# Kernel tuning notes

Hardware: AMD Instinct MI355X
Metric: run time of the kernel (lower is better)

## Reference

```python
import jax, jax.numpy as jnp
import numpy as np

B, T, NM = 128, 2048, 8  # batch, nSteps, nMaxwell


def setup_inputs() -> dict:
    key = jax.random.key(0)
    k1, k2, k3 = jax.random.split(key, 3)
    S_e = jax.random.normal(k1, (B, T, 3, 3), dtype=jnp.float32)
    # strictly increasing times per batch element
    dt = jax.random.uniform(k2, (B, T), minval=0.01, maxval=0.1, dtype=jnp.float32)
    t = jnp.cumsum(dt, axis=1)
    # [tau_1..tau_nM, g_infy, g_1..g_nM] -> last dim 2*NM + 1
    PronyParams = jax.random.uniform(k3, (B, T, 2 * NM + 1), minval=0.1, maxval=1.0, dtype=jnp.float32)
    return {"S_e": S_e, "t": t, "PronyParams": PronyParams}


def reference(S_e, t, PronyParams):
    """Viscoelastic 2nd Piola-Kirchhoff stress via recursive Prony update.

    S_e:         [B, T, 3, 3] instantaneous elastic stress
    t:           [B, T] time
    PronyParams: [B, T, 2*nM+1] (relaxation times tau then coefficients g)
    Returns (S, S_infy, Q_sum), each [B, T, 3, 3].
    """
    nM = PronyParams.shape[-1] // 2
    tau = PronyParams[..., :nM]                      # [B,T,nM]
    g = PronyParams[..., nM:]                        # [B,T,nM+1]
    g = g / jnp.sum(g, axis=-1, keepdims=True)
    g_infy = g[..., 0:1]                             # [B,T,1]
    g_i = g[..., 1:]                                 # [B,T,nM]

    Bsz = S_e.shape[0]
    # time-major scan inputs
    xs = (
        jnp.swapaxes(t, 0, 1),      # [T,B]
        jnp.swapaxes(S_e, 0, 1),    # [T,B,3,3]
        jnp.swapaxes(tau, 0, 1),    # [T,B,nM]
        jnp.swapaxes(g_i, 0, 1),    # [T,B,nM]
    )
    init = (
        jnp.zeros((Bsz, nM, 3, 3), S_e.dtype),  # Q_0
        -t[:, 1],                                # t_prev (as in original initializer)
        jnp.zeros((Bsz, 3, 3), S_e.dtype),       # S_prev
        tau[:, 0],
        g_i[:, 0],
    )

    def step(carry, x):
        Q_p, t_p, S_p, tau_p, g_p = carry
        t_c, S_c, tau_c, g_c = x
        g_bar = 0.5 * (g_c + g_p)                 # [B,nM]
        tau_bar = 0.5 * (tau_c + tau_p)           # [B,nM]
        dt = (t_c - t_p)[:, None]                 # [B,1]
        e = jnp.exp(-0.5 * dt / tau_bar)          # exp(-dt/(2 tau_bar))
        term1 = (e * e)[..., None, None]          # exp(-dt/tau_bar), [B,nM,1,1]
        term2 = (e * g_bar)[..., None, None]      # [B,nM,1,1]
        dS = (S_c - S_p)[:, None]                 # [B,1,3,3]
        Q = term1 * Q_p + term2 * dS              # [B,nM,3,3]
        return (Q, t_c, S_c, tau_c, g_c), Q

    _, Qs = jax.lax.scan(step, init, xs)          # [T,B,nM,3,3]
    Q_sum = jnp.swapaxes(jnp.sum(Qs, axis=2), 0, 1)  # [B,T,3,3]
    S_infy = g_infy[..., None] * S_e              # [B,T,1,1] * [B,T,3,3]
    S = S_infy + Q_sum
    return (S, S_infy, Q_sum)
```

## Files before the change

### kernel.cpp

```cpp
#include <hip/hip_runtime.h>

#define T_LEN 2048
#define NMODE 8
#define NPP   17

template <int L, int G>
__global__ __launch_bounds__(256, 8)
void aggK(const float* __restrict__ Se,
          const float* __restrict__ tt,
          const float* __restrict__ pp,
          float* __restrict__ agg,
          int B) {
    constexpr int NSTEP = G * L;
    constexpr int TILES = T_LEN / NSTEP;
    constexpr int RW    = NSTEP + 1;
    constexpr int NT    = 256;
    constexpr int AC_K  = L * 16 + 4;
    constexpr int OV_R  = 0;
    constexpr int OV_P  = G * 72;
    static_assert(OV_P + G * 8 <= G * AC_K, "overlay fits");
    constexpr int O_INV = G * AC_K;
    constexpr int TOTAL = O_INV + RW;

    __shared__ __align__(16) float sm[TOTAL];
    float* s_AC  = sm;
    float* s_R   = sm + OV_R;
    float* s_P   = sm + OV_P;
    float* s_inv = sm + O_INV;

    const int tid  = threadIdx.x;
    const int b    = blockIdx.x / (TILES - 1);
    const int tile = blockIdx.x % (TILES - 1);

    const int base = tile * NSTEP;
    const int off  = (base == 0) ? 0 : 1;
    const int r0   = (base == 0) ? 0 : base - 1;

    const float* ppb = pp + ((size_t)b * T_LEN + r0) * NPP;
    const float* ttb = tt + (size_t)b * T_LEN + r0;

    for (int i = tid; i < RW; i += NT) {
        const float* gp = ppb + i * NPP + 8;
        float gs = 0.f;
        #pragma unroll
        for (int k = 0; k < 9; ++k) gs += gp[k];
        s_inv[i] = __builtin_amdgcn_rcpf(gs);
    }
    __syncthreads();

    for (int i = tid; i < NSTEP * 8; i += NT) {
        int m  = i & 7;
        int ts = i >> 3;
        int rc = ts + off;
        bool first = (base == 0) && (ts == 0);
        int rp = first ? rc : rc - 1;
        float tau_c = ppb[rc * NPP + m];
        float tau_p = ppb[rp * NPP + m];
        float gqh_c = 0.5f * ppb[rc * NPP + 9 + m] * s_inv[rc];
        float gqh_p = 0.5f * ppb[rp * NPP + 9 + m] * s_inv[rp];
        float t_c = ttb[rc];
        float t_p = first ? -ttb[1] : ttb[rp];
        float ee  = __expf((t_p - t_c) * __builtin_amdgcn_rcpf(tau_c + tau_p));
        int kk = ts / L, sl = ts % L;
        s_AC[kk * AC_K + sl * 16 + m]     = ee * ee;
        s_AC[kk * AC_K + sl * 16 + 8 + m] = ee * (gqh_c + gqh_p);
    }
    __syncthreads();

    float Q[8] = {0,0,0,0,0,0,0,0};
    float cumA_c = 1.f;
    if (tid < 72) {
        const int k = tid / 9;
        const int e = tid - k * 9;
        const float* Sg = Se + (size_t)b * T_LEN * 9 + e;
        const int gbase = base + k * L;

        float dS[L];
        {
            float prev = (base == 0 && k == 0) ? 0.f
                                               : Sg[(size_t)(gbase - 1) * 9];
            #pragma unroll
            for (int s = 0; s < L; ++s) {
                float cur = Sg[(size_t)(gbase + s) * 9];
                dS[s] = cur - prev;
                prev = cur;
            }
        }

        const float4* acp = (const float4*)(s_AC + k * AC_K);
        #pragma unroll
        for (int s = 0; s < L; ++s) {
            float4 a0 = acp[4*s], a1 = acp[4*s+1];
            float4 c0v = acp[4*s+2], c1v = acp[4*s+3];
            float d = dS[s];
            Q[0] = a0.x*Q[0] + c0v.x*d;  Q[1] = a0.y*Q[1] + c0v.y*d;
            Q[2] = a0.z*Q[2] + c0v.z*d;  Q[3] = a0.w*Q[3] + c0v.w*d;
            Q[4] = a1.x*Q[4] + c1v.x*d;  Q[5] = a1.y*Q[5] + c1v.y*d;
            Q[6] = a1.z*Q[6] + c1v.z*d;  Q[7] = a1.w*Q[7] + c1v.w*d;
        }
    } else if (tid >= 192) {
        const int u = tid - 192;
        const int k = u >> 3;
        const int m = u & 7;
        #pragma unroll
        for (int s = 0; s < L; ++s)
            cumA_c *= s_AC[k * AC_K + s * 16 + m];
    }
    __syncthreads();

    if (tid < 72) {
        float4* r4 = (float4*)(s_R + 8 * tid);
        r4[0] = make_float4(Q[0], Q[1], Q[2], Q[3]);
        r4[1] = make_float4(Q[4], Q[5], Q[6], Q[7]);
    } else if (tid >= 192) {
        s_P[tid - 192] = cumA_c;
    }
    __syncthreads();

    if (tid < 72) {
        const int e = tid >> 3;
        const int m = tid & 7;
        float z = 0.f, pprod = 1.f;
        #pragma unroll
        for (int k = 0; k < G; ++k) {
            float Pk = s_P[k * 8 + m];
            z = Pk * z + s_R[k * 72 + tid];
            pprod *= Pk;
        }
        float* ap = agg + ((size_t)b * TILES + tile) * 80;
        ap[8 + tid] = z;
        if (e == 0) ap[m] = pprod;
    }
}

template <int L, int G>
__global__ __launch_bounds__(256, 8)
void finK(const float* __restrict__ Se,
          const float* __restrict__ tt,
          const float* __restrict__ pp,
          float* __restrict__ out,
          const float* __restrict__ agg,
          int B) {
    constexpr int NSTEP = G * L;
    constexpr int TILES = T_LEN / NSTEP;
    constexpr int RW    = NSTEP + 1;
    constexpr int NT    = 256;
    constexpr int SROW  = NSTEP + 4;
    constexpr int QT_SZ = 9 * SROW;
    constexpr int CA_K  = L * 8 + 4;
    constexpr int AC_K  = L * 16 + 4;
    constexpr int O_AC  = QT_SZ + G * CA_K;
    constexpr int OV_R  = 0;
    constexpr int OV_P  = G * 72;
    constexpr int OV_Z  = OV_P + G * 8;
    static_assert(OV_Z + G * 72 <= G * AC_K, "overlay fits");
    constexpr int O_INV = O_AC + G * AC_K;
    constexpr int O_GI  = O_INV + RW;
    constexpr int O_ZIN = O_GI + RW;
    constexpr int TOTAL = O_ZIN + 72;
    static_assert(TOTAL * 4 <= 20480, "LDS must allow 8 blocks/CU");
    static_assert(L == 16, "epilogue uses t>>4 / t&15");

    __shared__ __align__(16) float sm[TOTAL];
    float* s_qT  = sm;
    float* s_ca  = sm + QT_SZ;
    float* s_AC  = sm + O_AC;
    float* s_R   = sm + O_AC + OV_R;
    float* s_P   = sm + O_AC + OV_P;
    float* s_Z   = sm + O_AC + OV_Z;
    float* s_inv = sm + O_INV;
    float* s_gi  = sm + O_GI;
    float* s_Zin = sm + O_ZIN;

    const int tid  = threadIdx.x;
    const int b    = blockIdx.x / TILES;
    const int tile = blockIdx.x % TILES;

    const int base = tile * NSTEP;
    const int off  = (base == 0) ? 0 : 1;
    const int r0   = (base == 0) ? 0 : base - 1;

    const float* ppb = pp + ((size_t)b * T_LEN + r0) * NPP;
    const float* ttb = tt + (size_t)b * T_LEN + r0;

    if (tid < 72) {
        float zin = 0.f;
        if (tile > 0) {
            const int m = tid & 7;
            const float* ab = agg + (size_t)b * TILES * 80;
            float Pv[TILES - 1], Rv[TILES - 1];
            #pragma unroll
            for (int j = 0; j < TILES - 1; ++j) {
                if (j < tile) {
                    Pv[j] = ab[j * 80 + m];
                    Rv[j] = ab[j * 80 + 8 + tid];
                }
            }
            #pragma unroll
            for (int j = 0; j < TILES - 1; ++j)
                if (j < tile) zin = Pv[j] * zin + Rv[j];
        }
        s_Zin[tid] = zin;
    } else {
        int i = tid - 72;
        if (i < RW) {
            const float* gp = ppb + i * NPP + 8;
            float gs = 0.f;
            #pragma unroll
            for (int k = 0; k < 9; ++k) gs += gp[k];
            float iv = __builtin_amdgcn_rcpf(gs);
            s_inv[i] = iv;
            s_gi[i]  = gp[0] * iv;
        }
    }
    __syncthreads();

    for (int i = tid; i < NSTEP * 8; i += NT) {
        int m  = i & 7;
        int ts = i >> 3;
        int rc = ts + off;
        bool first = (base == 0) && (ts == 0);
        int rp = first ? rc : rc - 1;
        float tau_c = ppb[rc * NPP + m];
        float tau_p = ppb[rp * NPP + m];
        float gqh_c = 0.5f * ppb[rc * NPP + 9 + m] * s_inv[rc];
        float gqh_p = 0.5f * ppb[rp * NPP + 9 + m] * s_inv[rp];
        float t_c = ttb[rc];
        float t_p = first ? -ttb[1] : ttb[rp];
        float ee  = __expf((t_p - t_c) * __builtin_amdgcn_rcpf(tau_c + tau_p));
        int kk = ts / L, sl = ts % L;
        s_AC[kk * AC_K + sl * 16 + m]     = ee * ee;
        s_AC[kk * AC_K + sl * 16 + 8 + m] = ee * (gqh_c + gqh_p);
    }
    __syncthreads();

    const size_t nOut = (size_t)B * T_LEN * 9;
    float* o0 = out + ((size_t)b * T_LEN + base) * 9;
    float* o1 = o0 + nOut;
    float* o2 = o0 + 2 * nOut;
    const float4* sv4 = (const float4*)(Se + ((size_t)b * T_LEN + base) * 9);

    float Q[8] = {0,0,0,0,0,0,0,0};
    float cumA_c = 1.f;
    if (tid < 72) {
        const int k = tid / 9;
        const int e = tid - k * 9;
        const float* Sg = Se + (size_t)b * T_LEN * 9 + e;
        const int gbase = base + k * L;

        float dS[L];
        {
            float prev = (base == 0 && k == 0) ? 0.f
                                               : Sg[(size_t)(gbase - 1) * 9];
            #pragma unroll
            for (int s = 0; s < L; ++s) {
                float cur = Sg[(size_t)(gbase + s) * 9];
                dS[s] = cur - prev;
                prev = cur;
            }
        }

        const float4* acp = (const float4*)(s_AC + k * AC_K);
        #pragma unroll
        for (int s = 0; s < L; ++s) {
            float4 a0 = acp[4*s], a1 = acp[4*s+1];
            float4 c0v = acp[4*s+2], c1v = acp[4*s+3];
            float d = dS[s];
            Q[0] = a0.x*Q[0] + c0v.x*d;  Q[1] = a0.y*Q[1] + c0v.y*d;
            Q[2] = a0.z*Q[2] + c0v.z*d;  Q[3] = a0.w*Q[3] + c0v.w*d;
            Q[4] = a1.x*Q[4] + c1v.x*d;  Q[5] = a1.y*Q[5] + c1v.y*d;
            Q[6] = a1.z*Q[6] + c1v.z*d;  Q[7] = a1.w*Q[7] + c1v.w*d;
            float qs = ((Q[0]+Q[1])+(Q[2]+Q[3])) + ((Q[4]+Q[5])+(Q[6]+Q[7]));
            s_qT[e * SROW + (k * L + s)] = qs;
        }
    } else if (tid < 192) {
        for (int i4 = tid - 72; i4 < NSTEP * 9 / 4; i4 += 120) {
            float4 sv = sv4[i4];
            int i = i4 * 4;
            float f0 = s_gi[(i    ) / 9 + off] * sv.x;
            float f1 = s_gi[(i + 1) / 9 + off] * sv.y;
            float f2 = s_gi[(i + 2) / 9 + off] * sv.z;
            float f3 = s_gi[(i + 3) / 9 + off] * sv.w;
            ((float4*)o1)[i4] = make_float4(f0, f1, f2, f3);
        }
    } else {
        const int u = tid - 192;
        const int k = u >> 3;
        const int m = u & 7;
        #pragma unroll
        for (int s = 0; s < L; ++s) {
            cumA_c *= s_AC[k * AC_K + s * 16 + m];
            s_ca[k * CA_K + s * 8 + m] = cumA_c;
        }
    }
    __syncthreads();

    if (tid < 72) {
        float4* r4 = (float4*)(s_R + 8 * tid);
        r4[0] = make_float4(Q[0], Q[1], Q[2], Q[3]);
        r4[1] = make_float4(Q[4], Q[5], Q[6], Q[7]);
    } else if (tid >= 192) {
        s_P[tid - 192] = cumA_c;
    }
    __syncthreads();

    if (tid < 72) {
        const int m = tid & 7;
        float z = s_Zin[tid];
        #pragma unroll
        for (int k = 0; k < G; ++k) {
            s_Z[k * 72 + tid] = z;
            z = s_P[k * 8 + m] * z + s_R[k * 72 + tid];
        }
    }
    __syncthreads();

    for (int i4 = tid; i4 < NSTEP * 9 / 4; i4 += NT) {
        float4 sv = sv4[i4];
        const float svc[4] = {sv.x, sv.y, sv.z, sv.w};
        int i = i4 * 4;
        float q[4], f[4];
        #pragma unroll
        for (int j = 0; j < 4; ++j) {
            int idx = i + j;
            int t = idx / 9, e = idx - t * 9;
            int rc = t + off;
            int k = t >> 4, s = t & 15;
            const float4* ca4 = (const float4*)(s_ca + k * CA_K + s * 8);
            const float4* z4  = (const float4*)(s_Z + k * 72 + e * 8);
            float4 cA = ca4[0], cB = ca4[1];
            float4 zA = z4[0],  zB = z4[1];
            float cr = ((cA.x*zA.x + cA.y*zA.y) + (cA.z*zA.z + cA.w*zA.w))
                     + ((cB.x*zB.x + cB.y*zB.y) + (cB.z*zB.z + cB.w*zB.w));
            q[j] = s_qT[e * SROW + t] + cr;
            f[j] = s_gi[rc] * svc[j];
        }
        ((float4*)o2)[i4] = make_float4(q[0], q[1], q[2], q[3]);
        ((float4*)o0)[i4] = make_float4(f[0]+q[0], f[1]+q[1],
                                        f[2]+q[2], f[3]+q[3]);
    }
}

extern "C" void kernel_launch(void* const* d_in, const int* in_sizes, int n_in,
                              void* d_out, int out_size, void* d_ws, size_t ws_size,
                              hipStream_t stream) {
    const float* Se = (const float*)d_in[0];
    const float* tt = (const float*)d_in[1];
    const float* pp = (const float*)d_in[2];
    float* out = (float*)d_out;

    int B = in_sizes[1] / T_LEN;

    constexpr int L = 16;
    constexpr int G = 8;
    constexpr int NSTEP = G * L;
    constexpr int TILES = T_LEN / NSTEP;

    float* agg = (float*)d_ws;

    aggK<L, G><<<B * (TILES - 1), dim3(256), 0, stream>>>(
        Se, tt, pp, agg, B);
    finK<L, G><<<B * TILES, dim3(256), 0, stream>>>(
        Se, tt, pp, out, agg, B);
}
```

Measured before the change: 99.62 us.

## Fuse aggregate and finalize kernels into one cooperative kernel with grid sync

Merges the two-pass scan (per-tile aggregate, then finalize) into a single cooperative launch. Each tile's local recurrence, Q partials and cumulative decay factors stay in LDS across a grid-wide barrier, so the second pass no longer reloads and recomputes them. Output stores become nontemporal. The grid is B*16=2048 blocks, which needs 8 resident blocks per CU on 256 CUs. If the cooperative launch fails it falls back to the old two-kernel path, and the grid sync adds its own barrier cost.

```diff
diff --git a/kernel.cpp b/kernel.cpp
--- a/kernel.cpp
+++ b/kernel.cpp
@@ -1,36 +1,64 @@
 #include <hip/hip_runtime.h>
+#include <hip/hip_cooperative_groups.h>
 
 #define T_LEN 2048
 #define NMODE 8
 #define NPP   17
 
+namespace cg = cooperative_groups;
+
+typedef float f32x4 __attribute__((ext_vector_type(4)));
+
+static __device__ __forceinline__ void nt_store4(float* p, float a, float b,
+                                                 float c, float d) {
+    f32x4 v = {a, b, c, d};
+    __builtin_nontemporal_store(v, (f32x4*)p);
+}
+
 template <int L, int G>
 __global__ __launch_bounds__(256, 8)
-void aggK(const float* __restrict__ Se,
-          const float* __restrict__ tt,
-          const float* __restrict__ pp,
-          float* __restrict__ agg,
-          int B) {
+void fusedCoop(const float* __restrict__ Se,
+               const float* __restrict__ tt,
+               const float* __restrict__ pp,
+               float* __restrict__ out,
+               float* __restrict__ agg,
+               int B) {
     constexpr int NSTEP = G * L;
     constexpr int TILES = T_LEN / NSTEP;
     constexpr int RW    = NSTEP + 1;
     constexpr int NT    = 256;
+    constexpr int SROW  = NSTEP + 4;
+    constexpr int QT_SZ = 9 * SROW;
+    constexpr int CA_K  = L * 8 + 4;
     constexpr int AC_K  = L * 16 + 4;
-    constexpr int OV_R  = 0;
-    constexpr int OV_P  = G * 72;
-    static_assert(OV_P + G * 8 <= G * AC_K, "overlay fits");
-    constexpr int O_INV = G * AC_K;
-    constexpr int TOTAL = O_INV + RW;
+    constexpr int O_AC  = QT_SZ + G * CA_K;
+    constexpr int OV_ZREL = 0;
+    constexpr int OV_PP   = G * 72;
+    constexpr int OV_Z    = OV_PP + G * 8;
+    constexpr int OV_R    = OV_Z + G * 72;
+    constexpr int OV_P    = OV_R + G * 72;
+    static_assert(OV_P + G * 8 <= G * AC_K, "overlay fits in AC region");
+    constexpr int O_INV = O_AC + G * AC_K;
+    constexpr int O_GI  = O_INV + RW;
+    constexpr int TOTAL = O_GI + RW;
+    static_assert(TOTAL * 4 <= 20480, "LDS must allow 8 blocks/CU");
+    static_assert(L == 16, "epilogue uses t>>4 / t&15");
 
     __shared__ __align__(16) float sm[TOTAL];
-    float* s_AC  = sm;
-    float* s_R   = sm + OV_R;
-    float* s_P   = sm + OV_P;
-    float* s_inv = sm + O_INV;
+    float* s_qT   = sm;
+    float* s_ca   = sm + QT_SZ;
+    float* s_AC   = sm + O_AC;
+    float* s_Zrel = sm + O_AC + OV_ZREL;
+    float* s_Pp   = sm + O_AC + OV_PP;
+    float* s_Z    = sm + O_AC + OV_Z;
+    float* s_R    = sm + O_AC + OV_R;
+    float* s_P    = sm + O_AC + OV_P;
+    float* s_inv  = sm + O_INV;
+    float* s_gi   = sm + O_GI;
 
     const int tid  = threadIdx.x;
-    const int b    = blockIdx.x / (TILES - 1);
-    const int tile = blockIdx.x % (TILES - 1);
+    const int b    = blockIdx.x / TILES;
+    const int tile = blockIdx.x % TILES;
 
     const int base = tile * NSTEP;
     const int off  = (base == 0) ? 0 : 1;
@@ -44,7 +72,9 @@
         float gs = 0.f;
         #pragma unroll
         for (int k = 0; k < 9; ++k) gs += gp[k];
-        s_inv[i] = __builtin_amdgcn_rcpf(gs);
+        float iv = __builtin_amdgcn_rcpf(gs);
+        s_inv[i] = iv;
+        s_gi[i]  = gp[0] * iv;
     }
     __syncthreads();
 
@@ -67,6 +97,12 @@
     }
     __syncthreads();
 
+    const size_t nOut = (size_t)B * T_LEN * 9;
+    float* o0 = out + ((size_t)b * T_LEN + base) * 9;
+    float* o1 = o0 + nOut;
+    float* o2 = o0 + 2 * nOut;
+    const float4* sv4 = (const float4*)(Se + ((size_t)b * T_LEN + base) * 9);
+
     float Q[8] = {0,0,0,0,0,0,0,0};
     float cumA_c = 1.f;
     if (tid < 72) {
@@ -97,14 +133,28 @@
             Q[2] = a0.z*Q[2] + c0v.z*d;  Q[3] = a0.w*Q[3] + c0v.w*d;
             Q[4] = a1.x*Q[4] + c1v.x*d;  Q[5] = a1.y*Q[5] + c1v.y*d;
             Q[6] = a1.z*Q[6] + c1v.z*d;  Q[7] = a1.w*Q[7] + c1v.w*d;
-        }
-    } else if (tid >= 192) {
+            float qs = ((Q[0]+Q[1])+(Q[2]+Q[3])) + ((Q[4]+Q[5])+(Q[6]+Q[7]));
+            s_qT[e * SROW + (k * L + s)] = qs;
+        }
+    } else if (tid < 192) {
+        for (int i4 = tid - 72; i4 < NSTEP * 9 / 4; i4 += 120) {
+            float4 sv = sv4[i4];
+            int i = i4 * 4;
+            nt_store4(o1 + i,
+                      s_gi[(i    ) / 9 + off] * sv.x,
+                      s_gi[(i + 1) / 9 + off] * sv.y,
+                      s_gi[(i + 2) / 9 + off] * sv.z,
+                      s_gi[(i + 3) / 9 + off] * sv.w);
+        }
+    } else {
         const int u = tid - 192;
         const int k = u >> 3;
         const int m = u & 7;
         #pragma unroll
-        for (int s = 0; s < L; ++s)
+        for (int s = 0; s < L; ++s) {
             cumA_c *= s_AC[k * AC_K + s * 16 + m];
+            s_ca[k * CA_K + s * 8 + m] = cumA_c;
+        }
     }
     __syncthreads();
 
@@ -123,58 +173,100 @@
         float z = 0.f, pprod = 1.f;
         #pragma unroll
         for (int k = 0; k < G; ++k) {
+            s_Zrel[k * 72 + tid] = z;
+            if (e == 0) s_Pp[k * 8 + m] = pprod;
             float Pk = s_P[k * 8 + m];
             z = Pk * z + s_R[k * 72 + tid];
             pprod *= Pk;
         }
-        float* ap = agg + ((size_t)b * TILES + tile) * 80;
-        ap[8 + tid] = z;
-        if (e == 0) ap[m] = pprod;
+        if (tile != TILES - 1) {
+            float* ap = agg + ((size_t)b * TILES + tile) * 80;
+            __hip_atomic_store(ap + 8 + tid, z, __ATOMIC_RELAXED,
+                               __HIP_MEMORY_SCOPE_AGENT);
+            if (e == 0)
+                __hip_atomic_store(ap + m, pprod, __ATOMIC_RELAXED,
+                                   __HIP_MEMORY_SCOPE_AGENT);
+        }
+    }
+    asm volatile("s_waitcnt vmcnt(0)" ::: "memory");
+
+    cg::this_grid().sync();
+
+    if (tid < 72) {
+        const int m = tid & 7;
+        float zin = 0.f;
+        if (tile > 0) {
+            const float* ab = agg + (size_t)b * TILES * 80;
+            float Pv[TILES - 1], Rv[TILES - 1];
+            #pragma unroll
+            for (int j = 0; j < TILES - 1; ++j) {
+                if (j < tile) {
+                    Pv[j] = __hip_atomic_load(ab + j * 80 + m,
+                                              __ATOMIC_RELAXED,
+                                              __HIP_MEMORY_SCOPE_AGENT);
+                    Rv[j] = __hip_atomic_load(ab + j * 80 + 8 + tid,
+                                              __ATOMIC_RELAXED,
+                                              __HIP_MEMORY_SCOPE_AGENT);
+                }
+            }
+            #pragma unroll
+            for (int j = 0; j < TILES - 1; ++j)
+                if (j < tile) zin = Pv[j] * zin + Rv[j];
+        }
+        #pragma unroll
+        for (int k = 0; k < G; ++k)
+            s_Z[k * 72 + tid] = s_Pp[k * 8 + m] * zin + s_Zrel[k * 72 + tid];
+    }
+    __syncthreads();
+
+    for (int i4 = tid; i4 < NSTEP * 9 / 4; i4 += NT) {
+        float4 sv = sv4[i4];
+        const float svc[4] = {sv.x, sv.y, sv.z, sv.w};
+        int i = i4 * 4;
+        float q[4], f[4];
+        #pragma unroll
+        for (int j = 0; j < 4; ++j) {
+            int idx = i + j;
+            int t = idx / 9, e = idx - t * 9;
+            int rc = t + off;
+            int k = t >> 4, s = t & 15;
+            const float4* ca4 = (const float4*)(s_ca + k * CA_K + s * 8);
+            const float4* z4  = (const float4*)(s_Z + k * 72 + e * 8);
+            float4 cA = ca4[0], cB = ca4[1];
+            float4 zA = z4[0],  zB = z4[1];
+            float cr = ((cA.x*zA.x + cA.y*zA.y) + (cA.z*zA.z + cA.w*zA.w))
+                     + ((cB.x*zB.x + cB.y*zB.y) + (cB.z*zB.z + cB.w*zB.w));
+            q[j] = s_qT[e * SROW + t] + cr;
+            f[j] = s_gi[rc] * svc[j];
+        }
+        nt_store4(o2 + i, q[0], q[1], q[2], q[3]);
+        nt_store4(o0 + i, f[0]+q[0], f[1]+q[1], f[2]+q[2], f[3]+q[3]);
     }
 }
 
 template <int L, int G>
 __global__ __launch_bounds__(256, 8)
-void finK(const float* __restrict__ Se,
-          const float* __restrict__ tt,
-          const float* __restrict__ pp,
-          float* __restrict__ out,
-          const float* __restrict__ agg,
-          int B) {
+void aggK(const float* __restrict__ Se, const float* __restrict__ tt,
+          const float* __restrict__ pp, float* __restrict__ agg, int B) {
     constexpr int NSTEP = G * L;
     constexpr int TILES = T_LEN / NSTEP;
     constexpr int RW    = NSTEP + 1;
     constexpr int NT    = 256;
-    constexpr int SROW  = NSTEP + 4;
-    constexpr int QT_SZ = 9 * SROW;
-    constexpr int CA_K  = L * 8 + 4;
     constexpr int AC_K  = L * 16 + 4;
-    constexpr int O_AC  = QT_SZ + G * CA_K;
     constexpr int OV_R  = 0;
     constexpr int OV_P  = G * 72;
-    constexpr int OV_Z  = OV_P + G * 8;
-    static_assert(OV_Z + G * 72 <= G * AC_K, "overlay fits");
-    constexpr int O_INV = O_AC + G * AC_K;
-    constexpr int O_GI  = O_INV + RW;
-    constexpr int O_ZIN = O_GI + RW;
-    constexpr int TOTAL = O_ZIN + 72;
-    static_assert(TOTAL * 4 <= 20480, "LDS must allow 8 blocks/CU");
-    static_assert(L == 16, "epilogue uses t>>4 / t&15");
+    constexpr int O_INV = G * AC_K;
+    constexpr int TOTAL = O_INV + RW;
 
     __shared__ __align__(16) float sm[TOTAL];
-    float* s_qT  = sm;
-    float* s_ca  = sm + QT_SZ;
-    float* s_AC  = sm + O_AC;
-    float* s_R   = sm + O_AC + OV_R;
-    float* s_P   = sm + O_AC + OV_P;
-    float* s_Z   = sm + O_AC + OV_Z;
+    float* s_AC  = sm;
+    float* s_R   = sm + OV_R;
+    float* s_P   = sm + OV_P;
     float* s_inv = sm + O_INV;
-    float* s_gi  = sm + O_GI;
-    float* s_Zin = sm + O_ZIN;
 
     const int tid  = threadIdx.x;
-    const int b    = blockIdx.x / TILES;
-    const int tile = blockIdx.x % TILES;
+    const int b    = blockIdx.x / (TILES - 1);
+    const int tile = blockIdx.x % (TILES - 1);
 
     const int base = tile * NSTEP;
     const int off  = (base == 0) ? 0 : 1;
@@ -183,35 +275,12 @@
     const float* ppb = pp + ((size_t)b * T_LEN + r0) * NPP;
     const float* ttb = tt + (size_t)b * T_LEN + r0;
 
-    if (tid < 72) {
-        float zin = 0.f;
-        if (tile > 0) {
-            const int m = tid & 7;
-            const float* ab = agg + (size_t)b * TILES * 80;
-            float Pv[TILES - 1], Rv[TILES - 1];
-            #pragma unroll
-            for (int j = 0; j < TILES - 1; ++j) {
-                if (j < tile) {
-                    Pv[j] = ab[j * 80 + m];
-                    Rv[j] = ab[j * 80 + 8 + tid];
-                }
-            }
-            #pragma unroll
-            for (int j = 0; j < TILES - 1; ++j)
-                if (j < tile) zin = Pv[j] * zin + Rv[j];
-        }
-        s_Zin[tid] = zin;
-    } else {
-        int i = tid - 72;
-        if (i < RW) {
-            const float* gp = ppb + i * NPP + 8;
-            float gs = 0.f;
-            #pragma unroll
-            for (int k = 0; k < 9; ++k) gs += gp[k];
-            float iv = __builtin_amdgcn_rcpf(gs);
-            s_inv[i] = iv;
-            s_gi[i]  = gp[0] * iv;
-        }
+    for (int i = tid; i < RW; i += NT) {
+        const float* gp = ppb + i * NPP + 8;
+        float gs = 0.f;
+        #pragma unroll
+        for (int k = 0; k < 9; ++k) gs += gp[k];
+        s_inv[i] = __builtin_amdgcn_rcpf(gs);
     }
     __syncthreads();
 
@@ -234,6 +303,165 @@
     }
     __syncthreads();
 
+    float Q[8] = {0,0,0,0,0,0,0,0};
+    float cumA_c = 1.f;
+    if (tid < 72) {
+        const int k = tid / 9;
+        const int e = tid - k * 9;
+        const float* Sg = Se + (size_t)b * T_LEN * 9 + e;
+        const int gbase = base + k * L;
+        float dS[L];
+        {
+            float prev = (base == 0 && k == 0) ? 0.f
+                                               : Sg[(size_t)(gbase - 1) * 9];
+            #pragma unroll
+            for (int s = 0; s < L; ++s) {
+                float cur = Sg[(size_t)(gbase + s) * 9];
+                dS[s] = cur - prev;
+                prev = cur;
+            }
+        }
+        const float4* acp = (const float4*)(s_AC + k * AC_K);
+        #pragma unroll
+        for (int s = 0; s < L; ++s) {
+            float4 a0 = acp[4*s], a1 = acp[4*s+1];
+            float4 c0v = acp[4*s+2], c1v = acp[4*s+3];
+            float d = dS[s];
+            Q[0] = a0.x*Q[0] + c0v.x*d;  Q[1] = a0.y*Q[1] + c0v.y*d;
+            Q[2] = a0.z*Q[2] + c0v.z*d;  Q[3] = a0.w*Q[3] + c0v.w*d;
+            Q[4] = a1.x*Q[4] + c1v.x*d;  Q[5] = a1.y*Q[5] + c1v.y*d;
+            Q[6] = a1.z*Q[6] + c1v.z*d;  Q[7] = a1.w*Q[7] + c1v.w*d;
+        }
+    } else if (tid >= 192) {
+        const int u = tid - 192;
+        const int k = u >> 3;
+        const int m = u & 7;
+        #pragma unroll
+        for (int s = 0; s < L; ++s)
+            cumA_c *= s_AC[k * AC_K + s * 16 + m];
+    }
+    __syncthreads();
+
+    if (tid < 72) {
+        float4* r4 = (float4*)(s_R + 8 * tid);
+        r4[0] = make_float4(Q[0], Q[1], Q[2], Q[3]);
+        r4[1] = make_float4(Q[4], Q[5], Q[6], Q[7]);
+    } else if (tid >= 192) {
+        s_P[tid - 192] = cumA_c;
+    }
+    __syncthreads();
+
+    if (tid < 72) {
+        const int e = tid >> 3;
+        const int m = tid & 7;
+        float z = 0.f, pprod = 1.f;
+        #pragma unroll
+        for (int k = 0; k < G; ++k) {
+            float Pk = s_P[k * 8 + m];
+            z = Pk * z + s_R[k * 72 + tid];
+            pprod *= Pk;
+        }
+        float* ap = agg + ((size_t)b * TILES + tile) * 80;
+        ap[8 + tid] = z;
+        if (e == 0) ap[m] = pprod;
+    }
+}
+
+template <int L, int G>
+__global__ __launch_bounds__(256, 8)
+void finK(const float* __restrict__ Se, const float* __restrict__ tt,
+          const float* __restrict__ pp, float* __restrict__ out,
+          const float* __restrict__ agg, int B) {
+    constexpr int NSTEP = G * L;
+    constexpr int TILES = T_LEN / NSTEP;
+    constexpr int RW    = NSTEP + 1;
+    constexpr int NT    = 256;
+    constexpr int SROW  = NSTEP + 4;
+    constexpr int QT_SZ = 9 * SROW;
+    constexpr int CA_K  = L * 8 + 4;
+    constexpr int AC_K  = L * 16 + 4;
+    constexpr int O_AC  = QT_SZ + G * CA_K;
+    constexpr int OV_R  = 0;
+    constexpr int OV_P  = G * 72;
+    constexpr int OV_Z  = OV_P + G * 8;
+    constexpr int O_INV = O_AC + G * AC_K;
+    constexpr int O_GI  = O_INV + RW;
+    constexpr int O_ZIN = O_GI + RW;
+    constexpr int TOTAL = O_ZIN + 72;
+
+    __shared__ __align__(16) float sm[TOTAL];
+    float* s_qT  = sm;
+    float* s_ca  = sm + QT_SZ;
+    float* s_AC  = sm + O_AC;
+    float* s_R   = sm + O_AC + OV_R;
+    float* s_P   = sm + O_AC + OV_P;
+    float* s_Z   = sm + O_AC + OV_Z;
+    float* s_inv = sm + O_INV;
+    float* s_gi  = sm + O_GI;
+    float* s_Zin = sm + O_ZIN;
+
+    const int tid  = threadIdx.x;
+    const int b    = blockIdx.x / TILES;
+    const int tile = blockIdx.x % TILES;
+
+    const int base = tile * NSTEP;
+    const int off  = (base == 0) ? 0 : 1;
+    const int r0   = (base == 0) ? 0 : base - 1;
+
+    const float* ppb = pp + ((size_t)b * T_LEN + r0) * NPP;
+    const float* ttb = tt + (size_t)b * T_LEN + r0;
+
+    if (tid < 72) {
+        float zin = 0.f;
+        if (tile > 0) {
+            const int m = tid & 7;
+            const float* ab = agg + (size_t)b * TILES * 80;
+            float Pv[TILES - 1], Rv[TILES - 1];
+            #pragma unroll
+            for (int j = 0; j < TILES - 1; ++j) {
+                if (j < tile) {
+                    Pv[j] = ab[j * 80 + m];
+                    Rv[j] = ab[j * 80 + 8 + tid];
+                }
+            }
+            #pragma unroll
+            for (int j = 0; j < TILES - 1; ++j)
+                if (j < tile) zin = Pv[j] * zin + Rv[j];
+        }
+        s_Zin[tid] = zin;
+    } else {
+        int i = tid - 72;
+        if (i < RW) {
+            const float* gp = ppb + i * NPP + 8;
+            float gs = 0.f;
+            #pragma unroll
+            for (int k = 0; k < 9; ++k) gs += gp[k];
+            float iv = __builtin_amdgcn_rcpf(gs);
+            s_inv[i] = iv;
+            s_gi[i]  = gp[0] * iv;
+        }
+    }
+    __syncthreads();
+
+    for (int i = tid; i < NSTEP * 8; i += NT) {
+        int m  = i & 7;
+        int ts = i >> 3;
+        int rc = ts + off;
+        bool first = (base == 0) && (ts == 0);
+        int rp = first ? rc : rc - 1;
+        float tau_c = ppb[rc * NPP + m];
+        float tau_p = ppb[rp * NPP + m];
+        float gqh_c = 0.5f * ppb[rc * NPP + 9 + m] * s_inv[rc];
+        float gqh_p = 0.5f * ppb[rp * NPP + 9 + m] * s_inv[rp];
+        float t_c = ttb[rc];
+        float t_p = first ? -ttb[1] : ttb[rp];
+        float ee  = __expf((t_p - t_c) * __builtin_amdgcn_rcpf(tau_c + tau_p));
+        int kk = ts / L, sl = ts % L;
+        s_AC[kk * AC_K + sl * 16 + m]     = ee * ee;
+        s_AC[kk * AC_K + sl * 16 + 8 + m] = ee * (gqh_c + gqh_p);
+    }
+    __syncthreads();
+
     const size_t nOut = (size_t)B * T_LEN * 9;
     float* o0 = out + ((size_t)b * T_LEN + base) * 9;
     float* o1 = o0 + nOut;
@@ -247,7 +475,6 @@
         const int e = tid - k * 9;
         const float* Sg = Se + (size_t)b * T_LEN * 9 + e;
         const int gbase = base + k * L;
-
         float dS[L];
         {
             float prev = (base == 0 && k == 0) ? 0.f
@@ -259,7 +486,6 @@
                 prev = cur;
             }
         }
-
         const float4* acp = (const float4*)(s_AC + k * AC_K);
         #pragma unroll
         for (int s = 0; s < L; ++s) {
@@ -277,11 +503,11 @@
         for (int i4 = tid - 72; i4 < NSTEP * 9 / 4; i4 += 120) {
             float4 sv = sv4[i4];
             int i = i4 * 4;
-            float f0 = s_gi[(i    ) / 9 + off] * sv.x;
-            float f1 = s_gi[(i + 1) / 9 + off] * sv.y;
-            float f2 = s_gi[(i + 2) / 9 + off] * sv.z;
-            float f3 = s_gi[(i + 3) / 9 + off] * sv.w;
-            ((float4*)o1)[i4] = make_float4(f0, f1, f2, f3);
+            nt_store4(o1 + i,
+                      s_gi[(i    ) / 9 + off] * sv.x,
+                      s_gi[(i + 1) / 9 + off] * sv.y,
+                      s_gi[(i + 2) / 9 + off] * sv.z,
+                      s_gi[(i + 3) / 9 + off] * sv.w);
         }
     } else {
         const int u = tid - 192;
@@ -335,9 +561,8 @@
             q[j] = s_qT[e * SROW + t] + cr;
             f[j] = s_gi[rc] * svc[j];
         }
-        ((float4*)o2)[i4] = make_float4(q[0], q[1], q[2], q[3]);
-        ((float4*)o0)[i4] = make_float4(f[0]+q[0], f[1]+q[1],
-                                        f[2]+q[2], f[3]+q[3]);
+        nt_store4(o2 + i, q[0], q[1], q[2], q[3]);
+        nt_store4(o0 + i, f[0]+q[0], f[1]+q[1], f[2]+q[2], f[3]+q[3]);
     }
 }
 
@@ -358,8 +583,22 @@
 
     float* agg = (float*)d_ws;
 
-    aggK<L, G><<<B * (TILES - 1), dim3(256), 0, stream>>>(
-        Se, tt, pp, agg, B);
-    finK<L, G><<<B * TILES, dim3(256), 0, stream>>>(
-        Se, tt, pp, out, agg, B);
+    void* args[6];
+    args[0] = (void*)&Se;
+    args[1] = (void*)&tt;
+    args[2] = (void*)&pp;
+    args[3] = (void*)&out;
+    args[4] = (void*)&agg;
+    args[5] = (void*)&B;
+
+    hipError_t err = hipLaunchCooperativeKernel(
+        (const void*)fusedCoop<L, G>,
+        dim3(B * TILES), dim3(256), args, 0, stream);
+
+    if (err != hipSuccess) {
+        aggK<L, G><<<B * (TILES - 1), dim3(256), 0, stream>>>(
+            Se, tt, pp, agg, B);
+        finK<L, G><<<B * TILES, dim3(256), 0, stream>>>(
+            Se, tt, pp, out, agg, B);
+    }
 }
```

New measurement: 328.1 us. 3.29x slower.

## Stage Prony params and times in LDS, split mode recurrence across thread pairs

Applied to the files above, without the earlier changes.

Both kernels now copy the tile's PronyParams rows and time values into shared memory with coalesced loads, then compute normalisation and decay coefficients from LDS instead of scattered strided global reads. The per-element 8-mode recurrence is split across two threads of 4 modes each, combined with a lane shuffle. In the final kernel the aggregate prefix loads are issued before the staging copy to overlap latency. This adds an extra barrier and more LDS use, and leaves fewer threads for the S_infy output loop.

```diff
diff --git a/kernel.cpp b/kernel.cpp
--- a/kernel.cpp
+++ b/kernel.cpp
@@ -15,17 +15,23 @@
     constexpr int TILES = T_LEN / NSTEP;
     constexpr int RW    = NSTEP + 1;
     constexpr int NT    = 256;
+    constexpr int RAW_SZ = RW * NPP;
     constexpr int AC_K  = L * 16 + 4;
+    constexpr int O_T   = RAW_SZ;
+    constexpr int O_AC  = ((O_T + RW) + 3) & ~3;
     constexpr int OV_R  = 0;
     constexpr int OV_P  = G * 72;
     static_assert(OV_P + G * 8 <= G * AC_K, "overlay fits");
-    constexpr int O_INV = G * AC_K;
+    constexpr int O_INV = O_AC + G * AC_K;
     constexpr int TOTAL = O_INV + RW;
+    static_assert(TOTAL * 4 <= 20480, "8 blocks/CU");
 
     __shared__ __align__(16) float sm[TOTAL];
-    float* s_AC  = sm;
-    float* s_R   = sm + OV_R;
-    float* s_P   = sm + OV_P;
+    float* s_raw = sm;
+    float* s_t   = sm + O_T;
+    float* s_AC  = sm + O_AC;
+    float* s_R   = sm + O_AC + OV_R;
+    float* s_P   = sm + O_AC + OV_P;
     float* s_inv = sm + O_INV;
 
     const int tid  = threadIdx.x;
@@ -36,15 +42,19 @@
     const int off  = (base == 0) ? 0 : 1;
     const int r0   = (base == 0) ? 0 : base - 1;
 
-    const float* ppb = pp + ((size_t)b * T_LEN + r0) * NPP;
-    const float* ttb = tt + (size_t)b * T_LEN + r0;
-
-    for (int i = tid; i < RW; i += NT) {
-        const float* gp = ppb + i * NPP + 8;
+    {
+        const float* pr = pp + ((size_t)b * T_LEN + r0) * NPP;
+        for (int i = tid; i < RAW_SZ; i += NT) s_raw[i] = pr[i];
+        const float* tr = tt + (size_t)b * T_LEN + r0;
+        for (int i = tid; i < RW; i += NT) s_t[i] = tr[i];
+    }
+    __syncthreads();
+
+    if (tid < RW) {
         float gs = 0.f;
         #pragma unroll
-        for (int k = 0; k < 9; ++k) gs += gp[k];
-        s_inv[i] = __builtin_amdgcn_rcpf(gs);
+        for (int k = 8; k < NPP; ++k) gs += s_raw[tid * NPP + k];
+        s_inv[tid] = __builtin_amdgcn_rcpf(gs);
     }
     __syncthreads();
 
@@ -54,12 +64,12 @@
         int rc = ts + off;
         bool first = (base == 0) && (ts == 0);
         int rp = first ? rc : rc - 1;
-        float tau_c = ppb[rc * NPP + m];
-        float tau_p = ppb[rp * NPP + m];
-        float gqh_c = 0.5f * ppb[rc * NPP + 9 + m] * s_inv[rc];
-        float gqh_p = 0.5f * ppb[rp * NPP + 9 + m] * s_inv[rp];
-        float t_c = ttb[rc];
-        float t_p = first ? -ttb[1] : ttb[rp];
+        float tau_c = s_raw[rc * NPP + m];
+        float tau_p = s_raw[rp * NPP + m];
+        float gqh_c = 0.5f * s_raw[rc * NPP + 9 + m] * s_inv[rc];
+        float gqh_p = 0.5f * s_raw[rp * NPP + 9 + m] * s_inv[rp];
+        float t_c = s_t[rc];
+        float t_p = first ? -s_t[1] : s_t[rp];
         float ee  = __expf((t_p - t_c) * __builtin_amdgcn_rcpf(tau_c + tau_p));
         int kk = ts / L, sl = ts % L;
         s_AC[kk * AC_K + sl * 16 + m]     = ee * ee;
@@ -67,11 +77,13 @@
     }
     __syncthreads();
 
-    float Q[8] = {0,0,0,0,0,0,0,0};
+    float Q[4] = {0,0,0,0};
     float cumA_c = 1.f;
-    if (tid < 72) {
-        const int k = tid / 9;
-        const int e = tid - k * 9;
+    if (tid < 144) {
+        const int u = tid >> 1;
+        const int h = tid & 1;
+        const int k = u / 9;
+        const int e = u - k * 9;
         const float* Sg = Se + (size_t)b * T_LEN * 9 + e;
         const int gbase = base + k * L;
 
@@ -90,13 +102,11 @@
         const float4* acp = (const float4*)(s_AC + k * AC_K);
         #pragma unroll
         for (int s = 0; s < L; ++s) {
-            float4 a0 = acp[4*s], a1 = acp[4*s+1];
-            float4 c0v = acp[4*s+2], c1v = acp[4*s+3];
+            float4 a = acp[4*s + h];
+            float4 c = acp[4*s + 2 + h];
             float d = dS[s];
-            Q[0] = a0.x*Q[0] + c0v.x*d;  Q[1] = a0.y*Q[1] + c0v.y*d;
-            Q[2] = a0.z*Q[2] + c0v.z*d;  Q[3] = a0.w*Q[3] + c0v.w*d;
-            Q[4] = a1.x*Q[4] + c1v.x*d;  Q[5] = a1.y*Q[5] + c1v.y*d;
-            Q[6] = a1.z*Q[6] + c1v.z*d;  Q[7] = a1.w*Q[7] + c1v.w*d;
+            Q[0] = a.x*Q[0] + c.x*d;  Q[1] = a.y*Q[1] + c.y*d;
+            Q[2] = a.z*Q[2] + c.z*d;  Q[3] = a.w*Q[3] + c.w*d;
         }
     } else if (tid >= 192) {
         const int u = tid - 192;
@@ -108,10 +118,8 @@
     }
     __syncthreads();
 
-    if (tid < 72) {
-        float4* r4 = (float4*)(s_R + 8 * tid);
-        r4[0] = make_float4(Q[0], Q[1], Q[2], Q[3]);
-        r4[1] = make_float4(Q[4], Q[5], Q[6], Q[7]);
+    if (tid < 144) {
+        *(float4*)(s_R + 4 * tid) = make_float4(Q[0], Q[1], Q[2], Q[3]);
     } else if (tid >= 192) {
         s_P[tid - 192] = cumA_c;
     }
@@ -149,25 +157,31 @@
     constexpr int QT_SZ = 9 * SROW;
     constexpr int CA_K  = L * 8 + 4;
     constexpr int AC_K  = L * 16 + 4;
-    constexpr int O_AC  = QT_SZ + G * CA_K;
+    constexpr int RAW_SZ = RW * NPP;
+    constexpr int UNION_SZ = (RAW_SZ > QT_SZ + G * CA_K) ? RAW_SZ
+                                                         : (QT_SZ + G * CA_K);
+    constexpr int O_AC  = UNION_SZ;
     constexpr int OV_R  = 0;
     constexpr int OV_P  = G * 72;
     constexpr int OV_Z  = OV_P + G * 8;
     static_assert(OV_Z + G * 72 <= G * AC_K, "overlay fits");
-    constexpr int O_INV = O_AC + G * AC_K;
+    constexpr int O_T   = O_AC + G * AC_K;
+    constexpr int O_INV = O_T + RW;
     constexpr int O_GI  = O_INV + RW;
     constexpr int O_ZIN = O_GI + RW;
     constexpr int TOTAL = O_ZIN + 72;
-    static_assert(TOTAL * 4 <= 20480, "LDS must allow 8 blocks/CU");
+    static_assert(TOTAL * 4 <= 20480, "8 blocks/CU");
     static_assert(L == 16, "epilogue uses t>>4 / t&15");
 
     __shared__ __align__(16) float sm[TOTAL];
+    float* s_raw = sm;
     float* s_qT  = sm;
     float* s_ca  = sm + QT_SZ;
     float* s_AC  = sm + O_AC;
     float* s_R   = sm + O_AC + OV_R;
     float* s_P   = sm + O_AC + OV_P;
     float* s_Z   = sm + O_AC + OV_Z;
+    float* s_t   = sm + O_T;
     float* s_inv = sm + O_INV;
     float* s_gi  = sm + O_GI;
     float* s_Zin = sm + O_ZIN;
@@ -180,38 +194,42 @@
     const int off  = (base == 0) ? 0 : 1;
     const int r0   = (base == 0) ? 0 : base - 1;
 
-    const float* ppb = pp + ((size_t)b * T_LEN + r0) * NPP;
-    const float* ttb = tt + (size_t)b * T_LEN + r0;
-
+    float Pv[TILES - 1], Rv[TILES - 1];
+    if (tid < 72 && tile > 0) {
+        const int m = tid & 7;
+        const float* ab = agg + (size_t)b * TILES * 80;
+        #pragma unroll
+        for (int j = 0; j < TILES - 1; ++j) {
+            if (j < tile) {
+                Pv[j] = ab[j * 80 + m];
+                Rv[j] = ab[j * 80 + 8 + tid];
+            }
+        }
+    }
+    {
+        const float* pr = pp + ((size_t)b * T_LEN + r0) * NPP;
+        for (int i = tid; i < RAW_SZ; i += NT) s_raw[i] = pr[i];
+        const float* tr = tt + (size_t)b * T_LEN + r0;
+        for (int i = tid; i < RW; i += NT) s_t[i] = tr[i];
+    }
     if (tid < 72) {
         float zin = 0.f;
         if (tile > 0) {
-            const int m = tid & 7;
-            const float* ab = agg + (size_t)b * TILES * 80;
-            float Pv[TILES - 1], Rv[TILES - 1];
-            #pragma unroll
-            for (int j = 0; j < TILES - 1; ++j) {
-                if (j < tile) {
-                    Pv[j] = ab[j * 80 + m];
-                    Rv[j] = ab[j * 80 + 8 + tid];
-                }
-            }
             #pragma unroll
             for (int j = 0; j < TILES - 1; ++j)
                 if (j < tile) zin = Pv[j] * zin + Rv[j];
         }
         s_Zin[tid] = zin;
-    } else {
-        int i = tid - 72;
-        if (i < RW) {
-            const float* gp = ppb + i * NPP + 8;
-            float gs = 0.f;
-            #pragma unroll
-            for (int k = 0; k < 9; ++k) gs += gp[k];
-            float iv = __builtin_amdgcn_rcpf(gs);
-            s_inv[i] = iv;
-            s_gi[i]  = gp[0] * iv;
-        }
+    }
+    __syncthreads();
+
+    if (tid < RW) {
+        float gs = 0.f;
+        #pragma unroll
+        for (int k = 8; k < NPP; ++k) gs += s_raw[tid * NPP + k];
+        float iv = __builtin_amdgcn_rcpf(gs);
+        s_inv[tid] = iv;
+        s_gi[tid]  = s_raw[tid * NPP + 8] * iv;
     }
     __syncthreads();
 
@@ -221,12 +239,12 @@
         int rc = ts + off;
         bool first = (base == 0) && (ts == 0);
         int rp = first ? rc : rc - 1;
-        float tau_c = ppb[rc * NPP + m];
-        float tau_p = ppb[rp * NPP + m];
-        float gqh_c = 0.5f * ppb[rc * NPP + 9 + m] * s_inv[rc];
-        float gqh_p = 0.5f * ppb[rp * NPP + 9 + m] * s_inv[rp];
-        float t_c = ttb[rc];
-        float t_p = first ? -ttb[1] : ttb[rp];
+        float tau_c = s_raw[rc * NPP + m];
+        float tau_p = s_raw[rp * NPP + m];
+        float gqh_c = 0.5f * s_raw[rc * NPP + 9 + m] * s_inv[rc];
+        float gqh_p = 0.5f * s_raw[rp * NPP + 9 + m] * s_inv[rp];
+        float t_c = s_t[rc];
+        float t_p = first ? -s_t[1] : s_t[rp];
         float ee  = __expf((t_p - t_c) * __builtin_amdgcn_rcpf(tau_c + tau_p));
         int kk = ts / L, sl = ts % L;
         s_AC[kk * AC_K + sl * 16 + m]     = ee * ee;
@@ -240,11 +258,13 @@
     float* o2 = o0 + 2 * nOut;
     const float4* sv4 = (const float4*)(Se + ((size_t)b * T_LEN + base) * 9);
 
-    float Q[8] = {0,0,0,0,0,0,0,0};
+    float Q[4] = {0,0,0,0};
     float cumA_c = 1.f;
-    if (tid < 72) {
-        const int k = tid / 9;
-        const int e = tid - k * 9;
+    if (tid < 144) {
+        const int u = tid >> 1;
+        const int h = tid & 1;
+        const int k = u / 9;
+        const int e = u - k * 9;
         const float* Sg = Se + (size_t)b * T_LEN * 9 + e;
         const int gbase = base + k * L;
 
@@ -263,18 +283,17 @@
         const float4* acp = (const float4*)(s_AC + k * AC_K);
         #pragma unroll
         for (int s = 0; s < L; ++s) {
-            float4 a0 = acp[4*s], a1 = acp[4*s+1];
-            float4 c0v = acp[4*s+2], c1v = acp[4*s+3];
+            float4 a = acp[4*s + h];
+            float4 c = acp[4*s + 2 + h];
             float d = dS[s];
-            Q[0] = a0.x*Q[0] + c0v.x*d;  Q[1] = a0.y*Q[1] + c0v.y*d;
-            Q[2] = a0.z*Q[2] + c0v.z*d;  Q[3] = a0.w*Q[3] + c0v.w*d;
-            Q[4] = a1.x*Q[4] + c1v.x*d;  Q[5] = a1.y*Q[5] + c1v.y*d;
-            Q[6] = a1.z*Q[6] + c1v.z*d;  Q[7] = a1.w*Q[7] + c1v.w*d;
-            float qs = ((Q[0]+Q[1])+(Q[2]+Q[3])) + ((Q[4]+Q[5])+(Q[6]+Q[7]));
-            s_qT[e * SROW + (k * L + s)] = qs;
+            Q[0] = a.x*Q[0] + c.x*d;  Q[1] = a.y*Q[1] + c.y*d;
+            Q[2] = a.z*Q[2] + c.z*d;  Q[3] = a.w*Q[3] + c.w*d;
+            float qh = (Q[0] + Q[1]) + (Q[2] + Q[3]);
+            float qs = qh + __shfl_xor(qh, 1);
+            if (h == 0) s_qT[e * SROW + (k * L + s)] = qs;
         }
     } else if (tid < 192) {
-        for (int i4 = tid - 72; i4 < NSTEP * 9 / 4; i4 += 120) {
+        for (int i4 = tid - 144; i4 < NSTEP * 9 / 4; i4 += 48) {
             float4 sv = sv4[i4];
             int i = i4 * 4;
             float f0 = s_gi[(i    ) / 9 + off] * sv.x;
@@ -295,10 +314,8 @@
     }
     __syncthreads();
 
-    if (tid < 72) {
-        float4* r4 = (float4*)(s_R + 8 * tid);
-        r4[0] = make_float4(Q[0], Q[1], Q[2], Q[3]);
-        r4[1] = make_float4(Q[4], Q[5], Q[6], Q[7]);
+    if (tid < 144) {
+        *(float4*)(s_R + 4 * tid) = make_float4(Q[0], Q[1], Q[2], Q[3]);
     } else if (tid >= 192) {
         s_P[tid - 192] = cumA_c;
     }
```

After: 107.6 us. 8.0% more time.
